# Optimization experiments

Measured on AMD Instinct MI355X. Metric: run time of the kernel, lower is better.

The kernel has to match this reference:

```python
import jax, jax.numpy as jnp
import numpy as np

# RVQECell configuration (matches init_kwargs)
I_SZ, W_SZ, STAGES, ORDER, DEGREE = 6, 12, 3, 2, 2
BIAS = float(np.pi / 2)
ANC = ORDER - 1                      # ancillas_for_order(order) = order - 1
N = I_SZ + W_SZ + ANC                # 19 qubits
B = 32
INOUT = list(range(I_SZ))            # lanes 0..5
WORK = list(range(I_SZ, I_SZ + W_SZ))  # lanes 6..17
C_CTRL = I_SZ + W_SZ - 1             # controls per neuron = 17


def setup_inputs() -> dict:
    key = jax.random.key(0)
    ks = jax.random.split(key, 9)
    s = 0.1  # small init keeps neuron angles in a well-conditioned range
    psi = jax.random.normal(ks[0], (B, 2 ** N), jnp.float32)
    psi = psi / jnp.linalg.norm(psi, axis=1, keepdims=True)  # normalized kets
    return {
        "batch": psi,
        "w_in1": jax.random.normal(ks[1], (W_SZ, C_CTRL), jnp.float32) * s,
        "w_in2": jax.random.normal(ks[2], (W_SZ, C_CTRL, C_CTRL), jnp.float32) * s,
        "w_u": jax.random.normal(ks[3], (STAGES, W_SZ), jnp.float32) * s,
        "w_k1": jax.random.normal(ks[4], (STAGES, W_SZ, C_CTRL), jnp.float32) * s,
        "w_k2": jax.random.normal(ks[5], (STAGES, W_SZ, C_CTRL, C_CTRL), jnp.float32) * s,
        "w_out1": jax.random.normal(ks[6], (I_SZ, C_CTRL), jnp.float32) * s,
        "w_out2": jax.random.normal(ks[7], (I_SZ, C_CTRL, C_CTRL), jnp.float32) * s,
        "inputs": jax.random.randint(ks[8], (B, I_SZ), 0, 2, dtype=jnp.int32),
    }


def _rot_y(state, lane, alpha):
    # real rotation [[cos a, -sin a], [sin a, cos a]] on qubit `lane`.
    ax = lane + 1  # +1 for batch axis; state shape [B] + [2]*N
    c, s = jnp.cos(alpha), jnp.sin(alpha)
    p0 = jax.lax.index_in_dim(state, 0, ax, keepdims=True)
    p1 = jax.lax.index_in_dim(state, 1, ax, keepdims=True)
    return jnp.concatenate([c * p0 - s * p1, s * p0 + c * p1], axis=ax)


def _neuron(state, outlane, th1, th2):
    # Fast (deterministic RUS) quantum neuron of given ORDER/DEGREE:
    # per control-basis-branch rotation of `outlane` by alpha(x),
    # phi(x) = bias + sum_i th1_i x_i + sum_{i<j} th2_ij x_i x_j (degree 2),
    # alpha = q^(order-1)(phi), q(t) = arctan(tan(t)^2), stable via arctan2.
    controls = [l for l in range(I_SZ + W_SZ) if l != outlane]
    Cn = len(controls)
    x = jnp.arange(2 ** Cn)
    shifts = jnp.arange(Cn - 1, -1, -1)
    bits = ((x[:, None] >> shifts[None, :]) & 1).astype(state.dtype)  # [2^Cn, Cn]
    phi = BIAS + bits @ th1
    if DEGREE >= 2:
        phi = phi + jnp.einsum('xi,ij,xj->x', bits, jnp.triu(th2, 1), bits)
    alpha = phi
    for _ in range(ORDER - 1):
        alpha = jnp.arctan2(jnp.sin(alpha) ** 2, jnp.cos(alpha) ** 2)
    shape = [1] + [2 if l in controls else 1 for l in range(N)]
    return _rot_y(state, outlane, alpha.reshape(shape))


def _bitflip(state_flat, inputs):
    # Vectorized batched BitFlipLayer: X on inout lane i where inputs[b,i]==1,
    # i.e. permute amplitudes by XOR of the flip mask (lane 0 most significant).
    shifts = (N - 1) - jnp.arange(I_SZ)
    f = jnp.sum(inputs.astype(jnp.int32) << shifts[None, :], axis=1)  # [B]
    idx = jnp.arange(2 ** N, dtype=jnp.int32)[None, :] ^ f[:, None]
    return jnp.take_along_axis(state_flat, idx, axis=1)


def reference(batch, w_in1, w_in2, w_u, w_k1, w_k2, w_out1, w_out2, inputs):
    psi = _bitflip(batch, inputs).reshape((B,) + (2,) * N)
    # input layer: one neuron per workspace lane
    for j, out in enumerate(WORK):
        psi = _neuron(psi, out, w_in1[j], w_in2[j])
    # kernel layer: stages x (UnitaryLayer(workspace) + neurons)
    for st in range(STAGES):
        for j, lane in enumerate(WORK):
            psi = _rot_y(psi, lane, w_u[st, j])
        for j, out in enumerate(WORK):
            psi = _neuron(psi, out, w_k1[st, j], w_k2[st, j])
    psi = _bitflip(psi.reshape(B, -1), inputs).reshape((B,) + (2,) * N)
    # output layer: one neuron per inout lane
    for j, out in enumerate(INOUT):
        psi = _neuron(psi, out, w_out1[j], w_out2[j])
    # measurement probabilities over inout lanes: marginal of |amp|^2
    probs = jnp.sum(psi ** 2, axis=tuple(range(1 + I_SZ, 1 + N))).reshape(B, -1)
    return probs, psi.reshape(B, -1)
```

## Files before the change

### kernel.cpp

```cpp
#include <hip/hip_runtime.h>
#include <math.h>


#define BIAS_F 1.57079632679489662f

typedef float v4f __attribute__((ext_vector_type(4)));

__device__ __forceinline__ float4 ntload4(const float* p) {
    v4f v = __builtin_nontemporal_load((const v4f*)p);
    return make_float4(v.x, v.y, v.z, v.w);
}
__device__ __forceinline__ void ntstore4(float* p, float4 f) {
    v4f v = {f.x, f.y, f.z, f.w};
    __builtin_nontemporal_store(v, (v4f*)p);
}

__device__ __forceinline__ int SW(int i) { return i ^ ((i >> 3) & 0x1C); }
__device__ __forceinline__ float4 ldsld4(const float* st, int i) {
    return *(const float4*)&st[SW(i)];
}
__device__ __forceinline__ void ldsst4(float* st, int i, float4 v) {
    *(float4*)&st[SW(i)] = v;
}

#define LD2(p) (*(const float2*)(p))
#define LD4(p) (*(const float4*)(p))

__device__ __forceinline__ void rot4(float4& A, float4& B, float4 e) {
    float ax = A.x, ay = A.y, az = A.z, aw = A.w;
    A.x = e.x * ax - e.y * B.x;  B.x = e.y * ax + e.x * B.x;
    A.y = e.x * ay - e.y * B.y;  B.y = e.y * ay + e.x * B.y;
    A.z = e.z * az - e.w * B.z;  B.z = e.w * az + e.z * B.z;
    A.w = e.z * aw - e.w * B.w;  B.w = e.w * aw + e.z * B.w;
}
__device__ __forceinline__ void rotq(float4& P, float c, float s) {
    float px = P.x, py = P.y;
    P.x = c * px - s * P.z;  P.z = s * px + c * P.z;
    P.y = c * py - s * P.w;  P.w = s * py + c * P.w;
}


__global__ __launch_bounds__(256) void tables_kernel(
    const float* __restrict__ w_in1, const float* __restrict__ w_in2,
    const float* __restrict__ w_k1,  const float* __restrict__ w_k2,
    const float* __restrict__ w_out1, const float* __restrict__ w_out2,
    float* __restrict__ tab)
{
    const int n = blockIdx.y;
    const int hi = blockIdx.x;
    const int tid = threadIdx.x;
    const float* th1;
    const float* th2;
    if (n < 12)      { th1 = w_in1 + n * 17;         th2 = w_in2 + n * 289; }
    else if (n < 48) { th1 = w_k1 + (n - 12) * 17;   th2 = w_k2 + (n - 12) * 289; }
    else             { th1 = w_out1 + (n - 48) * 17; th2 = w_out2 + (n - 48) * 289; }

    float phi_hi = BIAS_F;
    float C[8];
#pragma unroll
    for (int a = 0; a < 8; ++a) C[a] = th1[9 + a];
#pragma unroll
    for (int i = 0; i < 9; ++i) {
        if ((hi >> (8 - i)) & 1) {
            float acc = th1[i];
#pragma unroll
            for (int j = i + 1; j < 9; ++j)
                if ((hi >> (8 - j)) & 1) acc += th2[i * 17 + j];
            phi_hi += acc;
#pragma unroll
            for (int a = 0; a < 8; ++a) C[a] += th2[i * 17 + 9 + a];
        }
    }

    float bt[8];
#pragma unroll
    for (int j = 0; j < 8; ++j) bt[j] = (float)((tid >> (7 - j)) & 1);
    float phi = phi_hi;
#pragma unroll
    for (int a = 0; a < 8; ++a) {
        float acc = C[a];
#pragma unroll
        for (int b2 = a + 1; b2 < 8; ++b2) acc += bt[b2] * th2[(9 + a) * 17 + 9 + b2];
        phi += bt[a] * acc;
    }

    float sp, cp;
    sincosf(phi, &sp, &cp);
    float c2 = cp * cp, s2 = sp * sp;
    float d = c2 * c2 + s2 * s2;
    float r = rsqrtf(d);
    r = r * (1.5f - 0.5f * d * r * r);
    float2* dst = (float2*)tab + ((size_t)n * 131072 + (size_t)((hi << 8) | tid));
    *dst = make_float2(c2 * r, s2 * r);
}

struct TabRegs { float4 r[12]; };

template <int PA>
__device__ __forceinline__ TabRegs tload_hi(const float* tA, const float* tB,
                                            const float* tC, int t8)
{
    const int lowb = PA - 4;
    const int low = t8 & ((1 << lowb) - 1);
    const int high = t8 >> lowb;
    const int x0 = (high << (PA - 1)) | (low << 1);
    const int dhi = (1 << PA) >> 2, dlo = (1 << PA) >> 3;
    TabRegs t;
    t.r[0]  = LD4(&tA[2 * x0]);            t.r[1]  = LD4(&tA[2 * (x0 + dlo)]);
    t.r[2]  = LD4(&tA[2 * (x0 + dhi)]);    t.r[3]  = LD4(&tA[2 * (x0 + dhi + dlo)]);
    t.r[4]  = LD4(&tB[2 * x0]);            t.r[5]  = LD4(&tB[2 * (x0 + dlo)]);
    t.r[6]  = LD4(&tB[2 * (x0 + dhi)]);    t.r[7]  = LD4(&tB[2 * (x0 + dhi + dlo)]);
    t.r[8]  = LD4(&tC[2 * x0]);            t.r[9]  = LD4(&tC[2 * (x0 + dlo)]);
    t.r[10] = LD4(&tC[2 * (x0 + dhi)]);    t.r[11] = LD4(&tC[2 * (x0 + dhi + dlo)]);
    return t;
}

__device__ __forceinline__ TabRegs tload_lo(const float* tA, const float* tB,
                                            const float* tC, int t8)
{
    const int x0 = t8 << 3;
    TabRegs t;
    t.r[0]  = LD4(&tA[2 * x0]);      t.r[1]  = LD4(&tA[2 * x0 + 4]);
    t.r[2]  = LD4(&tA[2 * x0 + 8]);  t.r[3]  = LD4(&tA[2 * x0 + 12]);
    t.r[4]  = LD4(&tB[2 * x0]);      t.r[5]  = LD4(&tB[2 * x0 + 4]);
    t.r[6]  = LD4(&tB[2 * x0 + 8]);  t.r[7]  = LD4(&tB[2 * x0 + 12]);
    t.r[8]  = LD4(&tC[2 * x0]);      t.r[9]  = LD4(&tC[2 * x0 + 4]);
    t.r[10] = LD4(&tC[2 * x0 + 8]);  t.r[11] = LD4(&tC[2 * x0 + 12]);
    return t;
}

template <int PA, bool NEUR, bool UNI>
__device__ __forceinline__ void compute_hi(float* l0, float* l1, int t8,
    const TabRegs& tr,
    float cA, float sA, float cB, float sB, float cC, float sC)
{
    const int lowb = PA - 4;
    const int low = t8 & ((1 << lowb) - 1);
    const int high = t8 >> lowb;
    const int i0 = (high << (PA + 1)) | (low << 2);
    const int oa = 1 << PA, ob = oa >> 1, oc = oa >> 2;
#pragma unroll
    for (int s = 0; s < 2; ++s) {
        float* sl = (s == 0) ? l0 : l1;
        float4 Q000 = ldsld4(sl, i0),            Q001 = ldsld4(sl, i0 + oc);
        float4 Q010 = ldsld4(sl, i0 + ob),       Q011 = ldsld4(sl, i0 + ob + oc);
        float4 Q100 = ldsld4(sl, i0 + oa),       Q101 = ldsld4(sl, i0 + oa + oc);
        float4 Q110 = ldsld4(sl, i0 + oa + ob),  Q111 = ldsld4(sl, i0 + oa + ob + oc);
        if (UNI || !NEUR) {
            float4 eA = make_float4(cA, sA, cA, sA);
            rot4(Q000, Q100, eA); rot4(Q001, Q101, eA);
            rot4(Q010, Q110, eA); rot4(Q011, Q111, eA);
            float4 eB = make_float4(cB, sB, cB, sB);
            rot4(Q000, Q010, eB); rot4(Q001, Q011, eB);
            rot4(Q100, Q110, eB); rot4(Q101, Q111, eB);
            float4 eC = make_float4(cC, sC, cC, sC);
            rot4(Q000, Q001, eC); rot4(Q010, Q011, eC);
            rot4(Q100, Q101, eC); rot4(Q110, Q111, eC);
        }
        if (NEUR) {
            rot4(Q000, Q100, tr.r[0]); rot4(Q001, Q101, tr.r[1]);
            rot4(Q010, Q110, tr.r[2]); rot4(Q011, Q111, tr.r[3]);
            rot4(Q000, Q010, tr.r[4]); rot4(Q001, Q011, tr.r[5]);
            rot4(Q100, Q110, tr.r[6]); rot4(Q101, Q111, tr.r[7]);
            rot4(Q000, Q001, tr.r[8]);  rot4(Q010, Q011, tr.r[9]);
            rot4(Q100, Q101, tr.r[10]); rot4(Q110, Q111, tr.r[11]);
        }
        ldsst4(sl, i0, Q000);            ldsst4(sl, i0 + oc, Q001);
        ldsst4(sl, i0 + ob, Q010);       ldsst4(sl, i0 + ob + oc, Q011);
        ldsst4(sl, i0 + oa, Q100);       ldsst4(sl, i0 + oa + oc, Q101);
        ldsst4(sl, i0 + oa + ob, Q110);  ldsst4(sl, i0 + oa + ob + oc, Q111);
    }
}

template <bool NEUR>
__device__ __forceinline__ void compute_lo(float* l0, float* l1, int t8,
    const TabRegs& tr,
    float cA, float sA, float cB, float sB, float cC, float sC)
{
    const int i0 = t8 << 5;
#pragma unroll
    for (int s = 0; s < 2; ++s) {
        float* sl = (s == 0) ? l0 : l1;
        float4 Q0 = ldsld4(sl, i0),      Q1 = ldsld4(sl, i0 + 4);
        float4 Q2 = ldsld4(sl, i0 + 8),  Q3 = ldsld4(sl, i0 + 12);
        float4 Q4 = ldsld4(sl, i0 + 16), Q5 = ldsld4(sl, i0 + 20);
        float4 Q6 = ldsld4(sl, i0 + 24), Q7 = ldsld4(sl, i0 + 28);
        if (NEUR) {
            rot4(Q0, Q2, tr.r[0]); rot4(Q1, Q3, tr.r[1]);
            rot4(Q4, Q6, tr.r[2]); rot4(Q5, Q7, tr.r[3]);
            rot4(Q0, Q1, tr.r[4]); rot4(Q2, Q3, tr.r[5]);
            rot4(Q4, Q5, tr.r[6]); rot4(Q6, Q7, tr.r[7]);
            rotq(Q0, tr.r[8].x,  tr.r[8].y);  rotq(Q1, tr.r[8].z,  tr.r[8].w);
            rotq(Q2, tr.r[9].x,  tr.r[9].y);  rotq(Q3, tr.r[9].z,  tr.r[9].w);
            rotq(Q4, tr.r[10].x, tr.r[10].y); rotq(Q5, tr.r[10].z, tr.r[10].w);
            rotq(Q6, tr.r[11].x, tr.r[11].y); rotq(Q7, tr.r[11].z, tr.r[11].w);
        } else {
            float4 eA = make_float4(cA, sA, cA, sA);
            rot4(Q0, Q2, eA); rot4(Q1, Q3, eA); rot4(Q4, Q6, eA); rot4(Q5, Q7, eA);
            float4 eB = make_float4(cB, sB, cB, sB);
            rot4(Q0, Q1, eB); rot4(Q2, Q3, eB); rot4(Q4, Q5, eB); rot4(Q6, Q7, eB);
            rotq(Q0, cC, sC); rotq(Q1, cC, sC); rotq(Q2, cC, sC); rotq(Q3, cC, sC);
            rotq(Q4, cC, sC); rotq(Q5, cC, sC); rotq(Q6, cC, sC); rotq(Q7, cC, sC);
        }
        ldsst4(sl, i0, Q0);      ldsst4(sl, i0 + 4, Q1);
        ldsst4(sl, i0 + 8, Q2);  ldsst4(sl, i0 + 12, Q3);
        ldsst4(sl, i0 + 16, Q4); ldsst4(sl, i0 + 20, Q5);
        ldsst4(sl, i0 + 24, Q6); ldsst4(sl, i0 + 28, Q7);
    }
}

__global__ __launch_bounds__(256, 1) void main_kernel(
    const float* __restrict__ batch, const float* __restrict__ w_u,
    const int* __restrict__ inputs, const float* __restrict__ tab,
    float* __restrict__ psi, float* __restrict__ probs)
{
    __shared__ __align__(16) float lds[2][8192];
    const int t8 = threadIdx.x;
    const int blk = blockIdx.x;
    const int xcd = blk & 7;
    const int vt = (xcd << 3) | ((blk >> 3) & 7);
    const int pair = blk >> 6;

    if (blk == 0) {
        float4 z = make_float4(0.f, 0.f, 0.f, 0.f);
        *(float4*)&probs[t8 * 8] = z;
        *(float4*)&probs[t8 * 8 + 4] = z;
    }

    int bb[2], uu[2];
#pragma unroll
    for (int s = 0; s < 2; ++s) {
        int b = pair * 2 + s;
        int fb = 0;
#pragma unroll
        for (int i = 0; i < 6; ++i) fb |= (inputs[b * 6 + i] & 1) << (5 - i);
        bb[s] = b; uu[s] = vt ^ fb;
        const float* src = batch + ((size_t)b << 19) + ((size_t)uu[s] << 13);
#pragma unroll
        for (int k = 0; k < 8; ++k) {
            int i4 = (k * 256 + t8) * 4;
            float4 v = ntload4(&src[i4]);
            *(float4*)&lds[s][SW(i4)] = v;
        }
    }
    float* l0 = lds[0];
    float* l1 = lds[1];

    const float* tb = tab + ((size_t)vt << 12);
#define TN(j) (tb + (size_t)(j) * 262144)
#define BAR __syncthreads()

    TabRegs A, B;
    A = tload_hi<12>(TN(0), TN(1), TN(2), t8);
    BAR;
    B = tload_hi<9>(TN(3), TN(4), TN(5), t8);
    compute_hi<12, true, false>(l0, l1, t8, A, 0,0,0,0,0,0);  BAR;
    A = tload_hi<6>(TN(6), TN(7), TN(8), t8);
    compute_hi<9, true, false>(l0, l1, t8, B, 0,0,0,0,0,0);   BAR;
    B = tload_lo(TN(9), TN(10), TN(11), t8);
    compute_hi<6, true, false>(l0, l1, t8, A, 0,0,0,0,0,0);   BAR;
    A = tload_hi<12>(TN(12), TN(13), TN(14), t8);
    compute_lo<true>(l0, l1, t8, B, 0,0,0,0,0,0);             BAR;

#pragma unroll 1
    for (int st2 = 0; st2 < 3; ++st2) {
        const float* wu = w_u + st2 * 12;
        const int nb = 12 + st2 * 12;
        float c0, s0, c1, s1, c2, s2;
        sincosf(wu[3], &s0, &c0); sincosf(wu[4], &s1, &c1); sincosf(wu[5], &s2, &c2);
        compute_hi<9, false, false>(l0, l1, t8, A, c0,s0, c1,s1, c2,s2);  BAR;
        sincosf(wu[6], &s0, &c0); sincosf(wu[7], &s1, &c1); sincosf(wu[8], &s2, &c2);
        compute_hi<6, false, false>(l0, l1, t8, A, c0,s0, c1,s1, c2,s2);  BAR;
        sincosf(wu[9], &s0, &c0); sincosf(wu[10], &s1, &c1); sincosf(wu[11], &s2, &c2);
        compute_lo<false>(l0, l1, t8, A, c0,s0, c1,s1, c2,s2);            BAR;

        sincosf(wu[0], &s0, &c0); sincosf(wu[1], &s1, &c1); sincosf(wu[2], &s2, &c2);
        B = tload_hi<9>(TN(nb+3), TN(nb+4), TN(nb+5), t8);
        compute_hi<12, true, true>(l0, l1, t8, A, c0,s0, c1,s1, c2,s2);   BAR;
        A = tload_hi<6>(TN(nb+6), TN(nb+7), TN(nb+8), t8);
        compute_hi<9, true, false>(l0, l1, t8, B, 0,0,0,0,0,0);           BAR;
        B = tload_lo(TN(nb+9), TN(nb+10), TN(nb+11), t8);
        compute_hi<6, true, false>(l0, l1, t8, A, 0,0,0,0,0,0);           BAR;
        if (st2 < 2)
            A = tload_hi<12>(TN(nb+12), TN(nb+13), TN(nb+14), t8);
        compute_lo<true>(l0, l1, t8, B, 0,0,0,0,0,0);                     BAR;
    }
#undef TN
#undef BAR

#pragma unroll
    for (int s = 0; s < 2; ++s) {
        float* dst = psi + ((size_t)bb[s] << 19) + ((size_t)uu[s] << 13);
#pragma unroll
        for (int k = 0; k < 8; ++k) {
            int i4 = (k * 256 + t8) * 4;
            float4 v = *(const float4*)&lds[s][SW(i4)];
            ntstore4(&dst[i4], v);
        }
    }
}

__global__ __launch_bounds__(256, 2) void out_kernel(
    const float* __restrict__ tab, float* __restrict__ psi,
    float* __restrict__ probs)
{
    __shared__ __align__(16) float ts[16384];
    const int tid = threadIdx.x;
    const int lane = tid & 63;
    const int wv = tid >> 6;
    const int b = blockIdx.x >> 5;
    const int c0 = (blockIdx.x & 31) << 8;
    float* gbase = psi + ((size_t)b << 19) + c0;

#pragma unroll
    for (int i = 0; i < 16; ++i) {
        int k = wv * 16 + i;
        float4 v = ntload4(&gbase[((size_t)k << 13) + lane * 4]);
        int f4 = lane ^ (k & 15);
        *(float4*)&ts[k * 256 + f4 * 4] = v;
    }
    __syncthreads();

    float a[64];
#pragma unroll
    for (int k = 0; k < 64; ++k) a[k] = ts[k * 256 + (tid ^ ((k & 15) << 2))];
    const int w12 = (c0 | tid) >> 1;

#define OSTAGE(J) { \
    const float* tj = tab + 2u * ((size_t)(48 + (J)) * 131072 + (size_t)w12); \
    _Pragma("unroll") \
    for (int h = 0; h < 2; ++h) { \
        float2 ev[16]; \
        _Pragma("unroll") \
        for (int m = 0; m < 16; ++m) ev[m] = LD2(&tj[(size_t)(h * 16 + m) << 13]); \
        _Pragma("unroll") \
        for (int m = 0; m < 16; ++m) { \
            const int mm = h * 16 + m; \
            const int q = 5 - (J); \
            const int k0 = ((mm >> q) << (q + 1)) | (mm & ((1 << q) - 1)); \
            const int k1 = k0 | (1 << q); \
            float2 e = ev[m]; \
            float A0 = a[k0], A1 = a[k1]; \
            a[k0] = e.x * A0 - e.y * A1; \
            a[k1] = e.y * A0 + e.x * A1; } } }
    OSTAGE(0) OSTAGE(1) OSTAGE(2) OSTAGE(3) OSTAGE(4) OSTAGE(5)
#undef OSTAGE

#pragma unroll
    for (int k = 0; k < 64; ++k) ts[k * 256 + (tid ^ ((k & 15) << 2))] = a[k];
    __syncthreads();

#pragma unroll
    for (int i = 0; i < 16; ++i) {
        int k = wv * 16 + i;
        int f4 = lane ^ (k & 15);
        float4 v = *(const float4*)&ts[k * 256 + f4 * 4];
        ntstore4(&gbase[((size_t)k << 13) + lane * 4], v);
    }

    const int k6 = tid & 63, seg = tid >> 6;
    float p = 0.f;
#pragma unroll
    for (int j = 0; j < 64; ++j) {
        int c = seg * 64 + ((j + k6) & 63);
        float v = ts[k6 * 256 + (c ^ ((k6 & 15) << 2))];
        p += v * v;
    }
    atomicAdd(&probs[b * 64 + k6], p);
}

extern "C" void kernel_launch(void* const* d_in, const int* in_sizes, int n_in,
                              void* d_out, int out_size, void* d_ws, size_t ws_size,
                              hipStream_t stream)
{
    const float* batch  = (const float*)d_in[0];
    const float* w_in1  = (const float*)d_in[1];
    const float* w_in2  = (const float*)d_in[2];
    const float* w_u    = (const float*)d_in[3];
    const float* w_k1   = (const float*)d_in[4];
    const float* w_k2   = (const float*)d_in[5];
    const float* w_out1 = (const float*)d_in[6];
    const float* w_out2 = (const float*)d_in[7];
    const int*   inputs = (const int*)d_in[8];
    float* probs = (float*)d_out;
    float* psi   = (float*)d_out + 2048;
    float* tab   = (float*)d_ws;

    tables_kernel<<<dim3(512, 54), 256, 0, stream>>>(w_in1, w_in2, w_k1, w_k2,
                                                     w_out1, w_out2, tab);
    main_kernel<<<1024, 256, 0, stream>>>(batch, w_u, inputs, tab, psi, probs);
    out_kernel<<<1024, 256, 0, stream>>>(tab, psi, probs);
}
```

Baseline: 368.0 us.

## Drop table-register double buffering to fit two blocks per CU

Replaces the two alternating table register sets (A/B) with one set loaded right before each compute phase, and raises launch bounds to allow two blocks per CU. This is meant to cut register pressure enough for two resident workgroups, so one block's table loads can overlap with another block's compute. In exchange, the in-block software prefetch of the next stage's tables is lost, so each phase waits on its own loads. The 64 KB of LDS per block must also still fit twice per CU.

```diff
diff --git a/kernel.cpp b/kernel.cpp
--- a/kernel.cpp
+++ b/kernel.cpp
@@ -209,7 +209,7 @@
     }
 }
 
-__global__ __launch_bounds__(256, 1) void main_kernel(
+__global__ __launch_bounds__(256, 2) void main_kernel(
     const float* __restrict__ batch, const float* __restrict__ w_u,
     const int* __restrict__ inputs, const float* __restrict__ tab,
     float* __restrict__ psi, float* __restrict__ probs)
@@ -250,40 +250,40 @@
 #define TN(j) (tb + (size_t)(j) * 262144)
 #define BAR __syncthreads()
 
-    TabRegs A, B;
-    A = tload_hi<12>(TN(0), TN(1), TN(2), t8);
+    TabRegs T;
+    T = tload_hi<12>(TN(0), TN(1), TN(2), t8);
     BAR;
-    B = tload_hi<9>(TN(3), TN(4), TN(5), t8);
-    compute_hi<12, true, false>(l0, l1, t8, A, 0,0,0,0,0,0);  BAR;
-    A = tload_hi<6>(TN(6), TN(7), TN(8), t8);
-    compute_hi<9, true, false>(l0, l1, t8, B, 0,0,0,0,0,0);   BAR;
-    B = tload_lo(TN(9), TN(10), TN(11), t8);
-    compute_hi<6, true, false>(l0, l1, t8, A, 0,0,0,0,0,0);   BAR;
-    A = tload_hi<12>(TN(12), TN(13), TN(14), t8);
-    compute_lo<true>(l0, l1, t8, B, 0,0,0,0,0,0);             BAR;
+    compute_hi<12, true, false>(l0, l1, t8, T, 0,0,0,0,0,0);  BAR;
+    T = tload_hi<9>(TN(3), TN(4), TN(5), t8);
+    compute_hi<9, true, false>(l0, l1, t8, T, 0,0,0,0,0,0);   BAR;
+    T = tload_hi<6>(TN(6), TN(7), TN(8), t8);
+    compute_hi<6, true, false>(l0, l1, t8, T, 0,0,0,0,0,0);   BAR;
+    T = tload_lo(TN(9), TN(10), TN(11), t8);
+    compute_lo<true>(l0, l1, t8, T, 0,0,0,0,0,0);             BAR;
 
 #pragma unroll 1
     for (int st2 = 0; st2 < 3; ++st2) {
         const float* wu = w_u + st2 * 12;
         const int nb = 12 + st2 * 12;
         float c0, s0, c1, s1, c2, s2;
+
+        T = tload_hi<12>(TN(nb+0), TN(nb+1), TN(nb+2), t8);
+
         sincosf(wu[3], &s0, &c0); sincosf(wu[4], &s1, &c1); sincosf(wu[5], &s2, &c2);
-        compute_hi<9, false, false>(l0, l1, t8, A, c0,s0, c1,s1, c2,s2);  BAR;
+        compute_hi<9, false, false>(l0, l1, t8, T, c0,s0, c1,s1, c2,s2);  BAR;
         sincosf(wu[6], &s0, &c0); sincosf(wu[7], &s1, &c1); sincosf(wu[8], &s2, &c2);
-        compute_hi<6, false, false>(l0, l1, t8, A, c0,s0, c1,s1, c2,s2);  BAR;
+        compute_hi<6, false, false>(l0, l1, t8, T, c0,s0, c1,s1, c2,s2);  BAR;
         sincosf(wu[9], &s0, &c0); sincosf(wu[10], &s1, &c1); sincosf(wu[11], &s2, &c2);
-        compute_lo<false>(l0, l1, t8, A, c0,s0, c1,s1, c2,s2);            BAR;
+        compute_lo<false>(l0, l1, t8, T, c0,s0, c1,s1, c2,s2);            BAR;
 
         sincosf(wu[0], &s0, &c0); sincosf(wu[1], &s1, &c1); sincosf(wu[2], &s2, &c2);
-        B = tload_hi<9>(TN(nb+3), TN(nb+4), TN(nb+5), t8);
-        compute_hi<12, true, true>(l0, l1, t8, A, c0,s0, c1,s1, c2,s2);   BAR;
-        A = tload_hi<6>(TN(nb+6), TN(nb+7), TN(nb+8), t8);
-        compute_hi<9, true, false>(l0, l1, t8, B, 0,0,0,0,0,0);           BAR;
-        B = tload_lo(TN(nb+9), TN(nb+10), TN(nb+11), t8);
-        compute_hi<6, true, false>(l0, l1, t8, A, 0,0,0,0,0,0);           BAR;
-        if (st2 < 2)
-            A = tload_hi<12>(TN(nb+12), TN(nb+13), TN(nb+14), t8);
-        compute_lo<true>(l0, l1, t8, B, 0,0,0,0,0,0);                     BAR;
+        compute_hi<12, true, true>(l0, l1, t8, T, c0,s0, c1,s1, c2,s2);   BAR;
+        T = tload_hi<9>(TN(nb+3), TN(nb+4), TN(nb+5), t8);
+        compute_hi<9, true, false>(l0, l1, t8, T, 0,0,0,0,0,0);           BAR;
+        T = tload_hi<6>(TN(nb+6), TN(nb+7), TN(nb+8), t8);
+        compute_hi<6, true, false>(l0, l1, t8, T, 0,0,0,0,0,0);           BAR;
+        T = tload_lo(TN(nb+9), TN(nb+10), TN(nb+11), t8);
+        compute_lo<true>(l0, l1, t8, T, 0,0,0,0,0,0);                     BAR;
     }
 #undef TN
 #undef BAR
```

Result: faster. 322.4 us (median of 2 runs) (-12.4%).
